# Performance work log

Measured on AMD Instinct MI355X. Metric: run time of the kernel, lower is better.

Reference implementation:

```python
import jax, jax.numpy as jnp
import numpy as np

N_NODES = 20000
N_EDGES = 200000
N_SEG = 16      # segments per operand
EXTENT = 32     # uniform segment extent
N_PATHS = 64
OP_SIZE = N_SEG * EXTENT  # 512


def setup_inputs() -> dict:
    key = jax.random.key(0)
    k1, k2, k3, k4, k5, k6 = jax.random.split(key, 6)
    x_nodes = jax.random.normal(k1, (N_NODES, OP_SIZE), dtype=jnp.float32)
    x_edges = jax.random.normal(k2, (N_EDGES, OP_SIZE), dtype=jnp.float32)
    path_coeffs = jax.random.normal(k3, (N_PATHS,), dtype=jnp.float32)
    src = jax.random.randint(k4, (N_EDGES,), 0, N_NODES, dtype=jnp.int64)
    dst = jax.random.randint(k5, (N_EDGES,), 0, N_NODES, dtype=jnp.int64)
    path_indices = jax.random.randint(k6, (N_PATHS, 3), 0, N_SEG, dtype=jnp.int64)
    return {"x_nodes": x_nodes, "x_edges": x_edges, "path_coeffs": path_coeffs,
            "src": src, "dst": dst, "path_indices": path_indices}


def reference(x_nodes, x_edges, path_coeffs, src, dst, path_indices):
    # Segmented polynomial, uniform 1d segments:
    #   for each edge b and path p with segment indices (i1, i2, i3) and coeff c_p:
    #     out[dst[b], i3, :] += c_p * x_nodes[src[b], i1, :] * x_edges[b, i2, :]
    n_nodes = x_nodes.shape[0]
    x1 = x_nodes[src].reshape(-1, N_SEG, EXTENT)        # [M, S, E] gather (input_indices)
    x2 = x_edges.reshape(-1, N_SEG, EXTENT)             # [M, S, E]
    i1, i2, i3 = path_indices[:, 0], path_indices[:, 1], path_indices[:, 2]
    # per-path segmented product with scalar coefficients: [M, P, E]
    contrib = path_coeffs[None, :, None] * x1[:, i1, :] * x2[:, i2, :]
    # segmented accumulation into output segments along axis 1
    edge_out = jnp.zeros((x2.shape[0], N_SEG, EXTENT), x_nodes.dtype).at[:, i3, :].add(contrib)
    # scatter_add edge outputs to nodes (output_indices)
    out = jnp.zeros((n_nodes, OP_SIZE), x_nodes.dtype).at[dst].add(edge_out.reshape(-1, OP_SIZE))
    return out
```

## Files before the change

### kernel.cpp

```cpp
#include <hip/hip_runtime.h>

#define N_NODES  20000
#define N_EDGES  200000
#define N_SEG    16
#define EXTENT   32
#define N_PATHS  64
#define OP_SIZE  (N_SEG * EXTENT)


__global__ void k_hist(const int* __restrict__ dst, int* __restrict__ offsets) {
    int e = blockIdx.x * blockDim.x + threadIdx.x;
    if (e < N_EDGES) atomicAdd(&offsets[dst[e]], 1);
}

__global__ void k_scan(int* __restrict__ offsets) {
    __shared__ int sums[256];
    const int T = 256;
    int tid = threadIdx.x;
    int chunk = (N_NODES + T - 1) / T;
    int lo = tid * chunk;
    int hi = lo + chunk; if (hi > N_NODES) hi = N_NODES;
    int s = 0;
    for (int i = lo; i < hi; ++i) s += offsets[i];
    sums[tid] = s;
    __syncthreads();
    if (tid == 0) {
        int acc = 0;
        for (int i = 0; i < T; ++i) { int v = sums[i]; sums[i] = acc; acc += v; }
    }
    __syncthreads();
    int acc = sums[tid];
    for (int i = lo; i < hi; ++i) { int v = offsets[i]; offsets[i] = acc; acc += v; }
}

__global__ void k_scatter(const int* __restrict__ dst, int* __restrict__ offsets,
                          int* __restrict__ edge_list) {
    int e = blockIdx.x * blockDim.x + threadIdx.x;
    if (e < N_EDGES) {
        int pos = atomicAdd(&offsets[dst[e]], 1);
        edge_list[pos] = e;
    }
}


__global__ __launch_bounds__(256) void k_main(
    const float* __restrict__ x_nodes, const float* __restrict__ x_edges,
    const float* __restrict__ path_coeffs, const int* __restrict__ src,
    const int* __restrict__ path_indices,
    const int* __restrict__ offsets, const int* __restrict__ edge_list,
    float* __restrict__ out)
{
    __shared__ float x1s[OP_SIZE];
    __shared__ float x2s[OP_SIZE];
    __shared__ float p_coef[N_PATHS];
    __shared__ int   p_i1[N_PATHS], p_i2[N_PATHS];
    __shared__ int   p_start[N_SEG + 1];

    const int tid = threadIdx.x;
    const int n   = blockIdx.x;

    if (tid < N_SEG) {
        int cnt = 0;
        for (int p = 0; p < N_PATHS; ++p)
            if (path_indices[p * 3 + 2] == tid) ++cnt;
        p_start[tid + 1] = cnt;
    }
    if (tid == 0) p_start[0] = 0;
    __syncthreads();
    if (tid == 0)
        for (int s = 0; s < N_SEG; ++s) p_start[s + 1] += p_start[s];
    __syncthreads();
    if (tid < N_SEG) {
        int w = p_start[tid];
        for (int p = 0; p < N_PATHS; ++p) {
            if (path_indices[p * 3 + 2] == tid) {
                p_i1[w]   = path_indices[p * 3 + 0];
                p_i2[w]   = path_indices[p * 3 + 1];
                p_coef[w] = path_coeffs[p];
                ++w;
            }
        }
    }
    __syncthreads();

    const int start = (n == 0) ? 0 : offsets[n - 1];
    const int end   = offsets[n];

    const int xl = tid & 31;
    const int s0 = tid >> 5;
    float acc0 = 0.f, acc1 = 0.f;

    for (int ei = start; ei < end; ++ei) {
        const int e  = edge_list[ei];
        const int sn = src[e];
        const float4* x1g = (const float4*)(x_nodes + (size_t)sn * OP_SIZE);
        const float4* x2g = (const float4*)(x_edges + (size_t)e  * OP_SIZE);
        if (tid < 128) ((float4*)x1s)[tid]       = x1g[tid];
        else           ((float4*)x2s)[tid - 128] = x2g[tid - 128];
        __syncthreads();

        {
            float a = 0.f;
            for (int k = p_start[s0]; k < p_start[s0 + 1]; ++k)
                a += p_coef[k] * x1s[p_i1[k] * EXTENT + xl] * x2s[p_i2[k] * EXTENT + xl];
            acc0 += a;
        }
        {
            const int s = s0 + 8;
            float a = 0.f;
            for (int k = p_start[s]; k < p_start[s + 1]; ++k)
                a += p_coef[k] * x1s[p_i1[k] * EXTENT + xl] * x2s[p_i2[k] * EXTENT + xl];
            acc1 += a;
        }
        __syncthreads();
    }

    const size_t ob = (size_t)n * OP_SIZE;
    out[ob + tid]       = acc0;
    out[ob + tid + 256] = acc1;
}


extern "C" void kernel_launch(void* const* d_in, const int* in_sizes, int n_in,
                              void* d_out, int out_size, void* d_ws, size_t ws_size,
                              hipStream_t stream) {
    const float* x_nodes      = (const float*)d_in[0];
    const float* x_edges      = (const float*)d_in[1];
    const float* path_coeffs  = (const float*)d_in[2];
    const int*   src          = (const int*)d_in[3];
    const int*   dst          = (const int*)d_in[4];
    const int*   path_indices = (const int*)d_in[5];
    float* out = (float*)d_out;

    int* offsets   = (int*)d_ws;
    int* edge_list = offsets + N_NODES;

    hipMemsetAsync(d_ws, 0, N_NODES * sizeof(int), stream);
    k_hist   <<<(N_EDGES + 255) / 256, 256, 0, stream>>>(dst, offsets);
    k_scan   <<<1, 256, 0, stream>>>(offsets);
    k_scatter<<<(N_EDGES + 255) / 256, 256, 0, stream>>>(dst, offsets, edge_list);
    k_main   <<<N_NODES, 256, 0, stream>>>(x_nodes, x_edges, path_coeffs, src,
                                           path_indices, offsets, edge_list, out);
}
```

Baseline: 790.9 us.

## Assign one wavefront per node with async LDS loads processing two edges per step

Each wavefront now owns one destination node instead of a whole block, and the block-wide __syncthreads per edge goes away. Edge data is loaded with direct global-to-LDS async copies, two edges per iteration, one per half-wave, and the halves are combined with a cross-lane shuffle at the end. Path metadata is precomputed once by a separate kernel into packed records read from global memory. The aim is to cut synchronisation overhead and raise memory-level parallelism, at the cost of more registers per thread and a reliance on the wait-count encoding being correct.

```diff
diff --git a/kernel.cpp b/kernel.cpp
--- a/kernel.cpp
+++ b/kernel.cpp
@@ -1,4 +1,5 @@
 #include <hip/hip_runtime.h>
+#include <stdint.h>
 
 #define N_NODES  20000
 #define N_EDGES  200000
@@ -42,82 +43,121 @@
     }
 }
 
+__global__ void k_paths(const int* __restrict__ path_indices,
+                        const float* __restrict__ path_coeffs,
+                        int* __restrict__ pstart, int2* __restrict__ rec) {
+    if (threadIdx.x == 0 && blockIdx.x == 0) {
+        int cnt[N_SEG + 1];
+        for (int i = 0; i <= N_SEG; ++i) cnt[i] = 0;
+        for (int p = 0; p < N_PATHS; ++p) cnt[path_indices[p * 3 + 2] + 1]++;
+        for (int i = 0; i < N_SEG; ++i) cnt[i + 1] += cnt[i];
+        for (int i = 0; i <= N_SEG; ++i) pstart[i] = cnt[i];
+        int cur[N_SEG];
+        for (int i = 0; i < N_SEG; ++i) cur[i] = cnt[i];
+        for (int p = 0; p < N_PATHS; ++p) {
+            int s3 = path_indices[p * 3 + 2];
+            int w = cur[s3]++;
+            int2 r;
+            r.x = ((path_indices[p * 3 + 0] * EXTENT) << 16) |
+                   (path_indices[p * 3 + 1] * EXTENT);
+            r.y = __float_as_int(path_coeffs[p]);
+            rec[w] = r;
+        }
+    }
+}
 
-__global__ __launch_bounds__(256) void k_main(
+
+__device__ __forceinline__ void async16(const float* g, float* l) {
+    __builtin_amdgcn_global_load_lds(
+        (const __attribute__((address_space(1))) uint32_t*)g,
+        (__attribute__((address_space(3))) uint32_t*)l, 16, 0, 0);
+}
+
+__global__ __launch_bounds__(256, 4) void k_main(
     const float* __restrict__ x_nodes, const float* __restrict__ x_edges,
-    const float* __restrict__ path_coeffs, const int* __restrict__ src,
-    const int* __restrict__ path_indices,
+    const int* __restrict__ src,
     const int* __restrict__ offsets, const int* __restrict__ edge_list,
+    const int* __restrict__ pstart, const int2* __restrict__ rec,
     float* __restrict__ out)
 {
-    __shared__ float x1s[OP_SIZE];
-    __shared__ float x2s[OP_SIZE];
-    __shared__ float p_coef[N_PATHS];
-    __shared__ int   p_i1[N_PATHS], p_i2[N_PATHS];
-    __shared__ int   p_start[N_SEG + 1];
+    __shared__ float lds[4 * 2048];
 
-    const int tid = threadIdx.x;
-    const int n   = blockIdx.x;
+    const int wid  = __builtin_amdgcn_readfirstlane(threadIdx.x >> 6);
+    const int lane = threadIdx.x & 63;
+    const int xl   = lane & 31;
+    const int h    = lane >> 5;
+    const int wb   = wid << 11;
 
-    if (tid < N_SEG) {
-        int cnt = 0;
-        for (int p = 0; p < N_PATHS; ++p)
-            if (path_indices[p * 3 + 2] == tid) ++cnt;
-        p_start[tid + 1] = cnt;
-    }
-    if (tid == 0) p_start[0] = 0;
-    __syncthreads();
-    if (tid == 0)
-        for (int s = 0; s < N_SEG; ++s) p_start[s + 1] += p_start[s];
-    __syncthreads();
-    if (tid < N_SEG) {
-        int w = p_start[tid];
-        for (int p = 0; p < N_PATHS; ++p) {
-            if (path_indices[p * 3 + 2] == tid) {
-                p_i1[w]   = path_indices[p * 3 + 0];
-                p_i2[w]   = path_indices[p * 3 + 1];
-                p_coef[w] = path_coeffs[p];
-                ++w;
-            }
-        }
-    }
-    __syncthreads();
+    const int n = blockIdx.x * 4 + wid;
+
+    int ks[N_SEG + 1];
+#pragma unroll
+    for (int i = 0; i <= N_SEG; ++i) ks[i] = pstart[i];
 
     const int start = (n == 0) ? 0 : offsets[n - 1];
     const int end   = offsets[n];
 
-    const int xl = tid & 31;
-    const int s0 = tid >> 5;
-    float acc0 = 0.f, acc1 = 0.f;
+    float acc[N_SEG];
+#pragma unroll
+    for (int s = 0; s < N_SEG; ++s) acc[s] = 0.f;
 
-    for (int ei = start; ei < end; ++ei) {
-        const int e  = edge_list[ei];
-        const int sn = src[e];
-        const float4* x1g = (const float4*)(x_nodes + (size_t)sn * OP_SIZE);
-        const float4* x2g = (const float4*)(x_edges + (size_t)e  * OP_SIZE);
-        if (tid < 128) ((float4*)x1s)[tid]       = x1g[tid];
-        else           ((float4*)x2s)[tid - 128] = x2g[tid - 128];
-        __syncthreads();
+    float* lA1 = lds + wb;
+    float* lA2 = lds + wb + 512;
+    float* lB1 = lds + wb + 1024;
+    float* lB2 = lds + wb + 1536;
+    const float* b1 = lds + wb + (h << 10);
+    const float* b2 = b1 + 512;
 
-        {
-            float a = 0.f;
-            for (int k = p_start[s0]; k < p_start[s0 + 1]; ++k)
-                a += p_coef[k] * x1s[p_i1[k] * EXTENT + xl] * x2s[p_i2[k] * EXTENT + xl];
-            acc0 += a;
+    for (int ei = start; ei < end; ei += 2) {
+        const int eA  = edge_list[ei];
+        const int snA = src[eA];
+        const float* gA1 = x_nodes + (size_t)snA * OP_SIZE + lane * 4;
+        const float* gA2 = x_edges + (size_t)eA  * OP_SIZE + lane * 4;
+        async16(gA1,       lA1);
+        async16(gA1 + 256, lA1 + 256);
+        async16(gA2,       lA2);
+        async16(gA2 + 256, lA2 + 256);
+
+        if (ei + 1 < end) {
+            const int eB  = edge_list[ei + 1];
+            const int snB = src[eB];
+            const float* gB1 = x_nodes + (size_t)snB * OP_SIZE + lane * 4;
+            const float* gB2 = x_edges + (size_t)eB  * OP_SIZE + lane * 4;
+            async16(gB1,       lB1);
+            async16(gB1 + 256, lB1 + 256);
+            async16(gB2,       lB2);
+            async16(gB2 + 256, lB2 + 256);
+        } else {
+            float4 z = make_float4(0.f, 0.f, 0.f, 0.f);
+            float4* zb = (float4*)lB1;
+            zb[lane]       = z;
+            zb[lane + 64]  = z;
+            zb[lane + 128] = z;
+            zb[lane + 192] = z;
         }
-        {
-            const int s = s0 + 8;
-            float a = 0.f;
-            for (int k = p_start[s]; k < p_start[s + 1]; ++k)
-                a += p_coef[k] * x1s[p_i1[k] * EXTENT + xl] * x2s[p_i2[k] * EXTENT + xl];
-            acc1 += a;
+
+        __builtin_amdgcn_s_waitcnt(0x0070);
+        __builtin_amdgcn_sched_barrier(0);
+
+#pragma unroll
+        for (int s = 0; s < N_SEG; ++s) {
+            float a = acc[s];
+            for (int k = ks[s]; k < ks[s + 1]; ++k) {
+                int2 r = rec[k];
+                a = fmaf(__int_as_float(r.y),
+                         b1[(r.x >> 16) + xl] * b2[(r.x & 0xffff) + xl], a);
+            }
+            acc[s] = a;
         }
-        __syncthreads();
     }
 
-    const size_t ob = (size_t)n * OP_SIZE;
-    out[ob + tid]       = acc0;
-    out[ob + tid + 256] = acc1;
+#pragma unroll
+    for (int s = 0; s < N_SEG; ++s) acc[s] += __shfl_xor(acc[s], 32);
+
+    float* row = out + (size_t)n * OP_SIZE;
+#pragma unroll
+    for (int j = 0; j < 8; ++j)
+        row[j * 64 + lane] = h ? acc[2 * j + 1] : acc[2 * j];
 }
 
 
@@ -132,13 +172,16 @@
     const int*   path_indices = (const int*)d_in[5];
     float* out = (float*)d_out;
 
-    int* offsets   = (int*)d_ws;
-    int* edge_list = offsets + N_NODES;
+    int*  offsets   = (int*)d_ws;
+    int*  edge_list = offsets + N_NODES;
+    int2* rec       = (int2*)(edge_list + N_EDGES);
+    int*  pstart    = (int*)(rec + N_PATHS);
 
-    hipMemsetAsync(d_ws, 0, N_NODES * sizeof(int), stream);
+    hipMemsetAsync(offsets, 0, N_NODES * sizeof(int), stream);
     k_hist   <<<(N_EDGES + 255) / 256, 256, 0, stream>>>(dst, offsets);
     k_scan   <<<1, 256, 0, stream>>>(offsets);
     k_scatter<<<(N_EDGES + 255) / 256, 256, 0, stream>>>(dst, offsets, edge_list);
-    k_main   <<<N_NODES, 256, 0, stream>>>(x_nodes, x_edges, path_coeffs, src,
-                                           path_indices, offsets, edge_list, out);
+    k_paths  <<<1, 64, 0, stream>>>(path_indices, path_coeffs, pstart, rec);
+    k_main   <<<N_NODES / 4, 256, 0, stream>>>(x_nodes, x_edges, src,
+                                               offsets, edge_list, pstart, rec, out);
 }
```

Result: faster. 768.7 us (-2.8%).
